# Kernel tuning notes

Measured on AMD Instinct MI355X. Metric: run time of the kernel, lower is better.

Reference implementation:

```python
import jax, jax.numpy as jnp
import numpy as np

N, E = 50000, 800000
F_IN, HID, NCLS = 128, 128, 64
EPS = 1e-6


def setup_inputs() -> dict:
    key = jax.random.key(0)
    ks = jax.random.split(key, 6)
    x = jax.random.normal(ks[0], (N, F_IN), dtype=jnp.float32)
    edge_index = jax.random.randint(ks[1], (2, E), 0, N, dtype=jnp.int32)
    # GCNConv glorot init
    W1 = jax.random.normal(ks[2], (F_IN, HID), dtype=jnp.float32) * np.sqrt(2.0 / (F_IN + HID))
    b1 = jnp.zeros((HID,), jnp.float32)
    gamma1 = jnp.ones((HID,), jnp.float32)
    beta1 = jnp.zeros((HID,), jnp.float32)
    W2 = jax.random.normal(ks[3], (HID, NCLS), dtype=jnp.float32) * np.sqrt(2.0 / (HID + NCLS))
    b2 = jnp.zeros((NCLS,), jnp.float32)
    return {"x": x, "edge_index": edge_index, "W1": W1, "b1": b1,
            "gamma1": gamma1, "beta1": beta1, "W2": W2, "b2": b2}


def _gcn_conv(x, src, dst, norm, W, b, n):
    # x' = A_hat @ (x W) + b, A_hat = D^-1/2 (A+I) D^-1/2
    h = x @ W                                   # [N, out]
    msg = h[src] * norm[:, None]                # [E+N, out] gather
    out = jax.ops.segment_sum(msg, dst, num_segments=n)  # scatter-add
    return out + b


def _layer_norm(h, gamma, beta):
    mu = jnp.mean(h, axis=-1, keepdims=True)
    var = jnp.mean(jnp.square(h - mu), axis=-1, keepdims=True)
    return (h - mu) * jax.lax.rsqrt(var + EPS) * gamma + beta


def reference(x, edge_index, W1, b1, gamma1, beta1, W2, b2):
    n = x.shape[0]
    loop = jnp.arange(n, dtype=edge_index.dtype)
    src = jnp.concatenate([edge_index[0], loop])  # add self loops
    dst = jnp.concatenate([edge_index[1], loop])
    deg = jax.ops.segment_sum(jnp.ones_like(dst, jnp.float32), dst, num_segments=n)
    dinv = jnp.where(deg > 0, jax.lax.rsqrt(deg), 0.0)
    norm = dinv[src] * dinv[dst]                 # [E+N]
    h = _gcn_conv(x, src, dst, norm, W1, b1, n)
    h = jax.nn.relu(_layer_norm(h, gamma1, beta1))
    out = _gcn_conv(h, src, dst, norm, W2, b2, n)
    return out
```

## Files before the change

kernel.cpp:

```cpp
#include <hip/hip_runtime.h>


typedef float f32x2 __attribute__((ext_vector_type(2)));
typedef float f32x4 __attribute__((ext_vector_type(4)));
typedef unsigned u32x4 __attribute__((ext_vector_type(4)));
typedef __bf16 bf16x8 __attribute__((ext_vector_type(8)));

__device__ __forceinline__ unsigned short f2bf(float f) {
    unsigned u = __float_as_uint(f);
    u += 0x7FFF + ((u >> 16) & 1);
    return (unsigned short)(u >> 16);
}
__device__ __forceinline__ float bfLo(unsigned g) { return __uint_as_float(g << 16); }
__device__ __forceinline__ float bfHi(unsigned g) { return __uint_as_float(g & 0xFFFF0000u); }

__global__ __launch_bounds__(256) void cvt_wi(const float* __restrict__ W1,
                                              const float* __restrict__ W2,
                                              unsigned short* __restrict__ W1t,
                                              unsigned short* __restrict__ W2t,
                                              int* __restrict__ cnt, int n) {
    int id = blockIdx.x * 256 + threadIdx.x;
    if (id < 128 * 128) {
        int c = id >> 7, k = id & 127;
        W1t[id] = f2bf(W1[k * 128 + c]);
    } else if (id < 128 * 128 + 64 * 128) {
        int j = id - 128 * 128;
        int c = j >> 7, k = j & 127;
        W2t[j] = f2bf(W2[k * 64 + c]);
    }
    if (id < n) cnt[id] = 0;
}

__global__ __launch_bounds__(256) void cvt_x(const float4* __restrict__ x4,
                                             uint4* __restrict__ xb4, int total) {
    int i = blockIdx.x * 256 + threadIdx.x;
    if (i >= total) return;
    float4 v0 = x4[2 * i], v1 = x4[2 * i + 1];
    uint4 o;
    o.x = (unsigned)f2bf(v0.x) | ((unsigned)f2bf(v0.y) << 16);
    o.y = (unsigned)f2bf(v0.z) | ((unsigned)f2bf(v0.w) << 16);
    o.z = (unsigned)f2bf(v1.x) | ((unsigned)f2bf(v1.y) << 16);
    o.w = (unsigned)f2bf(v1.z) | ((unsigned)f2bf(v1.w) << 16);
    xb4[i] = o;
}

__global__ void count_k(const int* __restrict__ dst, int* __restrict__ cnt,
                        int* __restrict__ rank, int e) {
    int i = blockIdx.x * blockDim.x + threadIdx.x;
    if (i < e) {
        int r = atomicAdd(&cnt[dst[i]], 1);
        __builtin_nontemporal_store(r, &rank[i]);
    }
}

__global__ __launch_bounds__(1024) void scan1_k(const int* __restrict__ cnt,
                                                int* __restrict__ incl,
                                                int* __restrict__ bsum, int n) {
    __shared__ int lds[1024];
    int t = threadIdx.x;
    int i = blockIdx.x * 1024 + t;
    int v = (i < n) ? ((cnt[i] + 7) & ~7) : 0;
    lds[t] = v;
    __syncthreads();
#pragma unroll
    for (int d = 1; d < 1024; d <<= 1) {
        int u = (t >= d) ? lds[t - d] : 0;
        __syncthreads();
        lds[t] += u;
        __syncthreads();
    }
    if (i < n) incl[i] = lds[t];
    if (t == 1023) bsum[blockIdx.x] = lds[1023];
}

__global__ __launch_bounds__(64) void scan2_k(const int* __restrict__ bsum,
                                              int* __restrict__ bpre, int nb) {
    int t = threadIdx.x;
    int v = (t < nb) ? bsum[t] : 0;
#pragma unroll
    for (int d = 1; d < 64; d <<= 1) {
        int u = __shfl_up(v, d);
        if (t >= d) v += u;
    }
    if (t < nb) bpre[t] = v - bsum[t];
}

__global__ __launch_bounds__(1024) void scan3_k(const int* __restrict__ cnt,
                                                const int* __restrict__ incl,
                                                const int* __restrict__ bpre,
                                                int* __restrict__ offs,
                                                float* __restrict__ dinv, int n) {
    int i = blockIdx.x * 1024 + threadIdx.x;
    if (i >= n) return;
    int c = cnt[i];
    int c8 = (c + 7) & ~7;
    int inc = incl[i] + bpre[blockIdx.x];
    offs[i] = inc - c8;
    dinv[i] = rsqrtf((float)(c + 1));
    if (i == n - 1) offs[n] = inc;
}

__global__ void fill_k(const int* __restrict__ src, const int* __restrict__ dst,
                       const int* __restrict__ rank, const int* __restrict__ offs,
                       const float* __restrict__ dinv,
                       unsigned* __restrict__ epk, int e) {
    int i = blockIdx.x * blockDim.x + threadIdx.x;
    if (i >= e) return;
    int s = src[i], d = dst[i];
    float w = dinv[s] * dinv[d];
    epk[offs[d] + rank[i]] = ((unsigned)s << 16) | (unsigned)f2bf(w);
}

template<int NT>
__global__ __launch_bounds__(256) void gemm_mfma(const uint4* __restrict__ Ab,
                                                 const uint4* __restrict__ Wt,
                                                 unsigned short* __restrict__ tab,
                                                 int n) {
    __shared__ uint4 As[64 * 16];
    int t = threadIdx.x;
    int r0 = blockIdx.x * 64;
    int rows = min(64, n - r0);
#pragma unroll
    for (int it = 0; it < 4; ++it) {
        int u = it * 256 + t;
        int row = u >> 4, s = u & 15;
        uint4 v = make_uint4(0u, 0u, 0u, 0u);
        if (row < rows) v = Ab[(size_t)(r0 + row) * 16 + s];
        As[row * 16 + (s ^ (row & 7))] = v;
    }
    __syncthreads();

    int wv = t >> 6, lane = t & 63;
    int arow = lane & 15;
    int kg = lane >> 4;
    int lrow = wv * 16 + arow;

    f32x4 acc[NT];
    f32x4 z = {0.f, 0.f, 0.f, 0.f};
#pragma unroll
    for (int j = 0; j < NT; ++j) acc[j] = z;

#pragma unroll
    for (int ks = 0; ks < 4; ++ks) {
        bf16x8 a = __builtin_bit_cast(bf16x8,
                       As[lrow * 16 + ((ks * 4 + kg) ^ (arow & 7))]);
#pragma unroll
        for (int tl = 0; tl < NT; ++tl) {
            bf16x8 b = __builtin_bit_cast(bf16x8,
                           Wt[(size_t)(tl * 16 + arow) * 16 + ks * 4 + kg]);
            acc[tl] = __builtin_amdgcn_mfma_f32_16x16x32_bf16(a, b, acc[tl], 0, 0, 0);
        }
    }

    int grow0 = r0 + wv * 16 + 4 * kg;
#pragma unroll
    for (int r = 0; r < 4; ++r) {
        int grow = grow0 + r;
        if (grow < n) {
            unsigned short* rowp = tab + (size_t)grow * (NT * 16) + arow;
#pragma unroll
            for (int tl = 0; tl < NT; ++tl)
                rowp[tl * 16] = f2bf(acc[tl][r]);
        }
    }
}

__global__ __launch_bounds__(256) void prop_ln(const unsigned* __restrict__ h0b,
                                               const int* __restrict__ offs,
                                               const unsigned* __restrict__ epk,
                                               const float* __restrict__ dinv,
                                               const float* __restrict__ b1,
                                               const float* __restrict__ gamma,
                                               const float* __restrict__ beta,
                                               unsigned* __restrict__ h1b, int n) {
    int wid = __builtin_amdgcn_readfirstlane((blockIdx.x * blockDim.x + threadIdx.x) >> 6);
    int lane = threadIdx.x & 63;
    if (wid >= n) return;
    float di = dinv[wid];
    unsigned self = h0b[(size_t)wid * 64 + lane];
    float a0 = bfLo(self) * di * di;
    float a1 = bfHi(self) * di * di;

    int s0 = offs[wid], s1 = offs[wid + 1];
    if (s0 < s1) {
        const u32x4* ep4 = (const u32x4*)(epk + s0);
        int nb8 = (s1 - s0) >> 3;
        u32x4 d0 = __builtin_nontemporal_load(ep4);
        u32x4 d1 = __builtin_nontemporal_load(ep4 + 1);
        for (int b = 0; b < nb8; ++b) {
            unsigned g0 = h0b[(size_t)(d0.x >> 16) * 64 + lane];
            unsigned g1 = h0b[(size_t)(d0.y >> 16) * 64 + lane];
            unsigned g2 = h0b[(size_t)(d0.z >> 16) * 64 + lane];
            unsigned g3 = h0b[(size_t)(d0.w >> 16) * 64 + lane];
            unsigned g4 = h0b[(size_t)(d1.x >> 16) * 64 + lane];
            unsigned g5 = h0b[(size_t)(d1.y >> 16) * 64 + lane];
            unsigned g6 = h0b[(size_t)(d1.z >> 16) * 64 + lane];
            unsigned g7 = h0b[(size_t)(d1.w >> 16) * 64 + lane];
            float w0 = bfLo(d0.x), w1 = bfLo(d0.y), w2 = bfLo(d0.z), w3 = bfLo(d0.w);
            float w4 = bfLo(d1.x), w5 = bfLo(d1.y), w6 = bfLo(d1.z), w7 = bfLo(d1.w);
            int bn = (b + 1 < nb8) ? b + 1 : 0;
            d0 = __builtin_nontemporal_load(ep4 + 2 * bn);
            d1 = __builtin_nontemporal_load(ep4 + 2 * bn + 1);
            a0 = fmaf(bfLo(g0), w0, a0); a1 = fmaf(bfHi(g0), w0, a1);
            a0 = fmaf(bfLo(g1), w1, a0); a1 = fmaf(bfHi(g1), w1, a1);
            a0 = fmaf(bfLo(g2), w2, a0); a1 = fmaf(bfHi(g2), w2, a1);
            a0 = fmaf(bfLo(g3), w3, a0); a1 = fmaf(bfHi(g3), w3, a1);
            a0 = fmaf(bfLo(g4), w4, a0); a1 = fmaf(bfHi(g4), w4, a1);
            a0 = fmaf(bfLo(g5), w5, a0); a1 = fmaf(bfHi(g5), w5, a1);
            a0 = fmaf(bfLo(g6), w6, a0); a1 = fmaf(bfHi(g6), w6, a1);
            a0 = fmaf(bfLo(g7), w7, a0); a1 = fmaf(bfHi(g7), w7, a1);
        }
    }

    a0 += b1[2 * lane];
    a1 += b1[2 * lane + 1];
    float sum = a0 + a1, sq = a0 * a0 + a1 * a1;
#pragma unroll
    for (int off = 32; off > 0; off >>= 1) {
        sum += __shfl_xor(sum, off);
        sq  += __shfl_xor(sq, off);
    }
    float mu  = sum * (1.f / 128.f);
    float var = fmaxf(sq * (1.f / 128.f) - mu * mu, 0.f);
    float rstd = rsqrtf(var + 1e-6f);
    float y0 = fmaxf((a0 - mu) * rstd * gamma[2 * lane] + beta[2 * lane], 0.f);
    float y1 = fmaxf((a1 - mu) * rstd * gamma[2 * lane + 1] + beta[2 * lane + 1], 0.f);
    unsigned pk = (unsigned)f2bf(y0) | ((unsigned)f2bf(y1) << 16);
    __builtin_nontemporal_store(pk, &h1b[(size_t)wid * 64 + lane]);
}

__global__ __launch_bounds__(256) void prop_out(const unsigned* __restrict__ h2b,
                                                const int* __restrict__ offs,
                                                const unsigned* __restrict__ epk,
                                                const float* __restrict__ dinv,
                                                const float* __restrict__ b2,
                                                float* __restrict__ out, int n) {
    int wid = __builtin_amdgcn_readfirstlane((blockIdx.x * blockDim.x + threadIdx.x) >> 6);
    int lane = threadIdx.x & 63;
    if (wid >= n) return;
    int es = lane >> 5, u = lane & 31;
    float di = dinv[wid];
    float a0 = 0.f, a1 = 0.f;
    if (es == 0) {
        unsigned self = h2b[(size_t)wid * 32 + u];
        a0 = bfLo(self) * di * di;
        a1 = bfHi(self) * di * di;
    }

    int s0 = offs[wid], s1 = offs[wid + 1];
    if (s0 < s1) {
        const u32x4* ep4 = (const u32x4*)(epk + s0);
        int nb8 = (s1 - s0) >> 3;
        u32x4 d0 = __builtin_nontemporal_load(ep4);
        u32x4 d1 = __builtin_nontemporal_load(ep4 + 1);
        for (int b = 0; b < nb8; ++b) {
            unsigned dd0 = es ? d0.y : d0.x;
            unsigned dd1 = es ? d0.w : d0.z;
            unsigned dd2 = es ? d1.y : d1.x;
            unsigned dd3 = es ? d1.w : d1.z;
            unsigned g0 = h2b[(size_t)(dd0 >> 16) * 32 + u];
            unsigned g1 = h2b[(size_t)(dd1 >> 16) * 32 + u];
            unsigned g2 = h2b[(size_t)(dd2 >> 16) * 32 + u];
            unsigned g3 = h2b[(size_t)(dd3 >> 16) * 32 + u];
            float w0 = bfLo(dd0), w1 = bfLo(dd1), w2 = bfLo(dd2), w3 = bfLo(dd3);
            int bn = (b + 1 < nb8) ? b + 1 : 0;
            d0 = __builtin_nontemporal_load(ep4 + 2 * bn);
            d1 = __builtin_nontemporal_load(ep4 + 2 * bn + 1);
            a0 = fmaf(bfLo(g0), w0, a0); a1 = fmaf(bfHi(g0), w0, a1);
            a0 = fmaf(bfLo(g1), w1, a0); a1 = fmaf(bfHi(g1), w1, a1);
            a0 = fmaf(bfLo(g2), w2, a0); a1 = fmaf(bfHi(g2), w2, a1);
            a0 = fmaf(bfLo(g3), w3, a0); a1 = fmaf(bfHi(g3), w3, a1);
        }
    }

    a0 += __shfl_xor(a0, 32);
    a1 += __shfl_xor(a1, 32);
    if (es == 0) {
        f32x2 o; o.x = a0 + b2[2 * u]; o.y = a1 + b2[2 * u + 1];
        __builtin_nontemporal_store(o, &((f32x2*)out)[(size_t)wid * 32 + u]);
    }
}

extern "C" void kernel_launch(void* const* d_in, const int* in_sizes, int n_in,
                              void* d_out, int out_size, void* d_ws, size_t ws_size,
                              hipStream_t stream) {
    const float* x     = (const float*)d_in[0];
    const int*   ei    = (const int*)d_in[1];
    const float* W1    = (const float*)d_in[2];
    const float* b1    = (const float*)d_in[3];
    const float* gam   = (const float*)d_in[4];
    const float* bet   = (const float*)d_in[5];
    const float* W2    = (const float*)d_in[6];
    const float* b2    = (const float*)d_in[7];
    float* out = (float*)d_out;

    int n = in_sizes[0] / 128;
    int e = in_sizes[1] / 2;
    const int* src = ei;
    const int* dst = ei + e;
    size_t ecap = (size_t)e + 8 * (size_t)n;

    char* p = (char*)d_ws;
    auto alloc = [&](size_t bytes) {
        void* q = (void*)p;
        p += (bytes + 255) & ~(size_t)255;
        return q;
    };
    int*            cnt   = (int*)alloc((size_t)n * 4);
    int*            offs  = (int*)alloc((size_t)(n + 1) * 4);
    int*            rank  = (int*)alloc((size_t)e * 4);
    float*          dinv  = (float*)alloc((size_t)n * 4);
    unsigned*       epk   = (unsigned*)alloc(ecap * 4);
    unsigned*       h0b   = (unsigned*)alloc((size_t)n * 64 * 4);
    char*           h1buf = (char*)alloc((size_t)n * 128 * 4);
    unsigned short* W1t   = (unsigned short*)alloc(128 * 128 * 2);
    unsigned short* W2t   = (unsigned short*)alloc(64 * 128 * 2);

    unsigned* h1b = (unsigned*)h1buf;
    uint4*    xb  = (uint4*)(h1buf + (size_t)n * 64 * 4);
    unsigned* h2b = h0b;
    int* incl = (int*)h0b;
    int* bsum = incl + n;
    int* bpre = bsum + 64;

    int nb = (n + 1023) / 1024;

    (void)hipMemsetAsync(epk, 0, ecap * 4, stream);
    cvt_wi<<<(n + 255) / 256, 256, 0, stream>>>(W1, W2, W1t, W2t, cnt, n);
    cvt_x<<<(n * 16 + 255) / 256, 256, 0, stream>>>((const float4*)x, xb, n * 16);
    count_k<<<(e + 255) / 256, 256, 0, stream>>>(dst, cnt, rank, e);
    scan1_k<<<nb, 1024, 0, stream>>>(cnt, incl, bsum, n);
    scan2_k<<<1, 64, 0, stream>>>(bsum, bpre, nb);
    scan3_k<<<nb, 1024, 0, stream>>>(cnt, incl, bpre, offs, dinv, n);
    fill_k<<<(e + 255) / 256, 256, 0, stream>>>(src, dst, rank, offs, dinv, epk, e);

    int gb = (n + 63) / 64;
    gemm_mfma<8><<<gb, 256, 0, stream>>>(xb, (const uint4*)W1t,
                                         (unsigned short*)h0b, n);
    prop_ln<<<(n + 3) / 4, 256, 0, stream>>>(h0b, offs, epk, dinv, b1, gam, bet, h1b, n);
    gemm_mfma<4><<<gb, 256, 0, stream>>>((const uint4*)h1b, (const uint4*)W2t,
                                         (unsigned short*)h2b, n);
    prop_out<<<(n + 3) / 4, 256, 0, stream>>>(h2b, offs, epk, dinv, b2, out, n);
}
```

Before: 172.3 us.

## Fuse scan passes with decoupled lookback, fold x conversion into GEMM, drop memset

Replaces the three-kernel prefix scan with a single kernel that chains block prefixes through a global state array using acquire/release atomics. The scan kernel now zeroes only the padding slots of each CSR row, which replaces the full memset of the edge buffer. The separate fp32-to-bf16 conversion of x is folded into the first GEMM's tile load. Together these cut several kernel launches and a full pass over x and the edge buffer, at the cost of a serial lookback chain across about 49 blocks and spin-waiting that relies on earlier blocks being scheduled first.

```diff
diff --git a/kernel.cpp b/kernel.cpp
--- a/kernel.cpp
+++ b/kernel.cpp
@@ -14,11 +14,12 @@
 __device__ __forceinline__ float bfLo(unsigned g) { return __uint_as_float(g << 16); }
 __device__ __forceinline__ float bfHi(unsigned g) { return __uint_as_float(g & 0xFFFF0000u); }
 
-__global__ __launch_bounds__(256) void cvt_wi(const float* __restrict__ W1,
-                                              const float* __restrict__ W2,
-                                              unsigned short* __restrict__ W1t,
-                                              unsigned short* __restrict__ W2t,
-                                              int* __restrict__ cnt, int n) {
+__global__ __launch_bounds__(256) void cvt_init(const float* __restrict__ W1,
+                                                const float* __restrict__ W2,
+                                                unsigned short* __restrict__ W1t,
+                                                unsigned short* __restrict__ W2t,
+                                                int* __restrict__ cnt,
+                                                int* __restrict__ bstate, int n) {
     int id = blockIdx.x * 256 + threadIdx.x;
     if (id < 128 * 128) {
         int c = id >> 7, k = id & 127;
@@ -29,19 +30,7 @@
         W2t[j] = f2bf(W2[k * 64 + c]);
     }
     if (id < n) cnt[id] = 0;
-}
-
-__global__ __launch_bounds__(256) void cvt_x(const float4* __restrict__ x4,
-                                             uint4* __restrict__ xb4, int total) {
-    int i = blockIdx.x * 256 + threadIdx.x;
-    if (i >= total) return;
-    float4 v0 = x4[2 * i], v1 = x4[2 * i + 1];
-    uint4 o;
-    o.x = (unsigned)f2bf(v0.x) | ((unsigned)f2bf(v0.y) << 16);
-    o.y = (unsigned)f2bf(v0.z) | ((unsigned)f2bf(v0.w) << 16);
-    o.z = (unsigned)f2bf(v1.x) | ((unsigned)f2bf(v1.y) << 16);
-    o.w = (unsigned)f2bf(v1.z) | ((unsigned)f2bf(v1.w) << 16);
-    xb4[i] = o;
+    if (id < 64) bstate[id] = -1;
 }
 
 __global__ void count_k(const int* __restrict__ dst, int* __restrict__ cnt,
@@ -53,14 +42,18 @@
     }
 }
 
-__global__ __launch_bounds__(1024) void scan1_k(const int* __restrict__ cnt,
-                                                int* __restrict__ incl,
-                                                int* __restrict__ bsum, int n) {
+__global__ __launch_bounds__(1024) void scan_k(const int* __restrict__ cnt,
+                                               int* __restrict__ offs,
+                                               float* __restrict__ dinv,
+                                               unsigned* __restrict__ epk,
+                                               int* __restrict__ bstate, int n) {
     __shared__ int lds[1024];
-    int t = threadIdx.x;
-    int i = blockIdx.x * 1024 + t;
-    int v = (i < n) ? ((cnt[i] + 7) & ~7) : 0;
-    lds[t] = v;
+    __shared__ int sPrefix;
+    int t = threadIdx.x, bid = blockIdx.x;
+    int i = bid * 1024 + t;
+    int c = (i < n) ? cnt[i] : 0;
+    int c8 = (c + 7) & ~7;
+    lds[t] = c8;
     __syncthreads();
 #pragma unroll
     for (int d = 1; d < 1024; d <<= 1) {
@@ -69,34 +62,28 @@
         lds[t] += u;
         __syncthreads();
     }
-    if (i < n) incl[i] = lds[t];
-    if (t == 1023) bsum[blockIdx.x] = lds[1023];
-}
-
-__global__ __launch_bounds__(64) void scan2_k(const int* __restrict__ bsum,
-                                              int* __restrict__ bpre, int nb) {
-    int t = threadIdx.x;
-    int v = (t < nb) ? bsum[t] : 0;
-#pragma unroll
-    for (int d = 1; d < 64; d <<= 1) {
-        int u = __shfl_up(v, d);
-        if (t >= d) v += u;
-    }
-    if (t < nb) bpre[t] = v - bsum[t];
-}
-
-__global__ __launch_bounds__(1024) void scan3_k(const int* __restrict__ cnt,
-                                                const int* __restrict__ incl,
-                                                const int* __restrict__ bpre,
-                                                int* __restrict__ offs,
-                                                float* __restrict__ dinv, int n) {
-    int i = blockIdx.x * 1024 + threadIdx.x;
+    if (t == 0) {
+        int pref = 0;
+        if (bid > 0) {
+            int v;
+            do {
+                v = __hip_atomic_load(&bstate[bid - 1], __ATOMIC_ACQUIRE,
+                                      __HIP_MEMORY_SCOPE_AGENT);
+            } while (v == -1);
+            pref = v;
+        }
+        __hip_atomic_store(&bstate[bid], pref + lds[1023], __ATOMIC_RELEASE,
+                           __HIP_MEMORY_SCOPE_AGENT);
+        sPrefix = pref;
+    }
+    __syncthreads();
     if (i >= n) return;
-    int c = cnt[i];
-    int c8 = (c + 7) & ~7;
-    int inc = incl[i] + bpre[blockIdx.x];
-    offs[i] = inc - c8;
+    int inc = sPrefix + lds[t];
+    int ex = inc - c8;
+    offs[i] = ex;
     dinv[i] = rsqrtf((float)(c + 1));
+    for (int j = c; j < c8; ++j)
+        __builtin_nontemporal_store(0u, &epk[ex + j]);
     if (i == n - 1) offs[n] = inc;
 }
 
@@ -111,8 +98,8 @@
     epk[offs[d] + rank[i]] = ((unsigned)s << 16) | (unsigned)f2bf(w);
 }
 
-template<int NT>
-__global__ __launch_bounds__(256) void gemm_mfma(const uint4* __restrict__ Ab,
+template<int NT, bool CVT>
+__global__ __launch_bounds__(256) void gemm_mfma(const void* __restrict__ Asrc,
                                                  const uint4* __restrict__ Wt,
                                                  unsigned short* __restrict__ tab,
                                                  int n) {
@@ -125,7 +112,19 @@
         int u = it * 256 + t;
         int row = u >> 4, s = u & 15;
         uint4 v = make_uint4(0u, 0u, 0u, 0u);
-        if (row < rows) v = Ab[(size_t)(r0 + row) * 16 + s];
+        if (row < rows) {
+            if constexpr (CVT) {
+                const float4* X4 = (const float4*)Asrc;
+                float4 a = X4[(size_t)(r0 + row) * 32 + 2 * s];
+                float4 b = X4[(size_t)(r0 + row) * 32 + 2 * s + 1];
+                v.x = (unsigned)f2bf(a.x) | ((unsigned)f2bf(a.y) << 16);
+                v.y = (unsigned)f2bf(a.z) | ((unsigned)f2bf(a.w) << 16);
+                v.z = (unsigned)f2bf(b.x) | ((unsigned)f2bf(b.y) << 16);
+                v.w = (unsigned)f2bf(b.z) | ((unsigned)f2bf(b.w) << 16);
+            } else {
+                v = ((const uint4*)Asrc)[(size_t)(r0 + row) * 16 + s];
+            }
+        }
         As[row * 16 + (s ^ (row & 7))] = v;
     }
     __syncthreads();
@@ -306,39 +305,31 @@
         p += (bytes + 255) & ~(size_t)255;
         return q;
     };
-    int*            cnt   = (int*)alloc((size_t)n * 4);
-    int*            offs  = (int*)alloc((size_t)(n + 1) * 4);
-    int*            rank  = (int*)alloc((size_t)e * 4);
-    float*          dinv  = (float*)alloc((size_t)n * 4);
-    unsigned*       epk   = (unsigned*)alloc(ecap * 4);
-    unsigned*       h0b   = (unsigned*)alloc((size_t)n * 64 * 4);
-    char*           h1buf = (char*)alloc((size_t)n * 128 * 4);
-    unsigned short* W1t   = (unsigned short*)alloc(128 * 128 * 2);
-    unsigned short* W2t   = (unsigned short*)alloc(64 * 128 * 2);
-
-    unsigned* h1b = (unsigned*)h1buf;
-    uint4*    xb  = (uint4*)(h1buf + (size_t)n * 64 * 4);
+    int*            cnt    = (int*)alloc((size_t)n * 4);
+    int*            offs   = (int*)alloc((size_t)(n + 1) * 4);
+    int*            rank   = (int*)alloc((size_t)e * 4);
+    float*          dinv   = (float*)alloc((size_t)n * 4);
+    int*            bstate = (int*)alloc(64 * 4);
+    unsigned*       epk    = (unsigned*)alloc(ecap * 4);
+    unsigned*       h0b    = (unsigned*)alloc((size_t)n * 64 * 4);
+    unsigned*       h1b    = (unsigned*)alloc((size_t)n * 64 * 4);
+    unsigned short* W1t    = (unsigned short*)alloc(128 * 128 * 2);
+    unsigned short* W2t    = (unsigned short*)alloc(64 * 128 * 2);
+
     unsigned* h2b = h0b;
-    int* incl = (int*)h0b;
-    int* bsum = incl + n;
-    int* bpre = bsum + 64;
 
     int nb = (n + 1023) / 1024;
 
-    (void)hipMemsetAsync(epk, 0, ecap * 4, stream);
-    cvt_wi<<<(n + 255) / 256, 256, 0, stream>>>(W1, W2, W1t, W2t, cnt, n);
-    cvt_x<<<(n * 16 + 255) / 256, 256, 0, stream>>>((const float4*)x, xb, n * 16);
+    cvt_init<<<(n + 255) / 256, 256, 0, stream>>>(W1, W2, W1t, W2t, cnt, bstate, n);
     count_k<<<(e + 255) / 256, 256, 0, stream>>>(dst, cnt, rank, e);
-    scan1_k<<<nb, 1024, 0, stream>>>(cnt, incl, bsum, n);
-    scan2_k<<<1, 64, 0, stream>>>(bsum, bpre, nb);
-    scan3_k<<<nb, 1024, 0, stream>>>(cnt, incl, bpre, offs, dinv, n);
+    scan_k<<<nb, 1024, 0, stream>>>(cnt, offs, dinv, epk, bstate, n);
     fill_k<<<(e + 255) / 256, 256, 0, stream>>>(src, dst, rank, offs, dinv, epk, e);
 
     int gb = (n + 63) / 64;
-    gemm_mfma<8><<<gb, 256, 0, stream>>>(xb, (const uint4*)W1t,
-                                         (unsigned short*)h0b, n);
+    gemm_mfma<8, true><<<gb, 256, 0, stream>>>(x, (const uint4*)W1t,
+                                               (unsigned short*)h0b, n);
     prop_ln<<<(n + 3) / 4, 256, 0, stream>>>(h0b, offs, epk, dinv, b1, gam, bet, h1b, n);
-    gemm_mfma<4><<<gb, 256, 0, stream>>>((const uint4*)h1b, (const uint4*)W2t,
-                                         (unsigned short*)h2b, n);
+    gemm_mfma<4, false><<<gb, 256, 0, stream>>>(h1b, (const uint4*)W2t,
+                                                (unsigned short*)h2b, n);
     prop_out<<<(n + 3) / 4, 256, 0, stream>>>(h2b, offs, epk, dinv, b2, out, n);
 }
```

After: 207.0 us. +20.1%, slower.
